# Kernel optimization log

Hardware: AMD Instinct MI355X
Metric: run time of the kernel (lower is better)

## Reference

```python
import jax, jax.numpy as jnp
import numpy as np

N_SU = 8
DATA_DIM = N_SU * N_SU - 1  # 63
BATCH = 1048576


def _gell_mann(n):
    """Generalized Gell-Mann matrices of su(n), Tr(L_a L_b) = 2 delta_ab."""
    mats = []
    for j in range(n):
        for k in range(j + 1, n):
            m = np.zeros((n, n), dtype=np.complex128); m[j, k] = 1.0; m[k, j] = 1.0
            mats.append(m)
            m = np.zeros((n, n), dtype=np.complex128); m[j, k] = -1.0j; m[k, j] = 1.0j
            mats.append(m)
    for l in range(1, n):
        m = np.zeros((n, n), dtype=np.complex128)
        c = np.sqrt(2.0 / (l * (l + 1)))
        for j in range(l):
            m[j, j] = c
        m[l, l] = -l * c
        mats.append(m)
    return np.stack(mats)


def _structure_const(n):
    """f_abc = Tr([L_a,L_b]L_c)/(4i), d_abc = Tr({L_a,L_b}L_c)/4 (both real)."""
    L = _gell_mann(n)                                  # (D, n, n)
    P = np.einsum('aij,bjk->abik', L, L)               # L_a L_b
    comm = P - P.transpose(1, 0, 2, 3)
    anti = P + P.transpose(1, 0, 2, 3)
    f = (np.einsum('abik,cki->abc', comm, L) / 4.0j).real
    d = (np.einsum('abik,cki->abc', anti, L) / 4.0).real
    return f.astype(np.float32), d.astype(np.float32)

F_CONST, D_CONST = _structure_const(N_SU)              # (D, D, D) each, compile-time constants
TRI = np.stack(np.triu_indices(DATA_DIM, 0))           # incl. diagonal
TRI1 = np.stack(np.triu_indices(DATA_DIM, 1))          # strict upper


def setup_inputs() -> dict:
    key = jax.random.key(0)
    k1, k2, k3, k4, k5 = jax.random.split(key, 5)
    D = DATA_DIM
    return {
        'x': jax.random.normal(k1, (BATCH, D), dtype=jnp.float32),
        'r_x': jax.random.uniform(k2, (D * (D + 1) // 2,), dtype=jnp.float32),
        'r_y': jax.random.uniform(k3, (D * (D - 1) // 2,), dtype=jnp.float32),
        'N': jax.random.uniform(k4, (1,), dtype=jnp.float32),
        'omega': jax.random.uniform(k5, (D,), dtype=jnp.float32),
    }


def _forward(x, r_x, r_y, N, omega):
    f = jnp.asarray(F_CONST)
    d = jnp.asarray(D_CONST)
    D = DATA_DIM
    # NOTE: faithful to the torch source, where `v_x = v_y = torch.zeros(...)`
    # aliases ONE tensor: r_y overwrites r_x on the strict upper triangle and
    # v_x is v_y, which makes c_im exactly zero.
    v = jnp.zeros((D, D), dtype=x.dtype)
    v = v.at[TRI[0], TRI[1]].set(r_x)
    v = v.at[TRI1[0], TRI1[1]].set(r_y)
    v_x = v
    v_y = v
    c_re = v_x.T @ v_x + v_y.T @ v_y                   # einsum('ki,kj->ij', v, v) x2
    c_re = c_re / jnp.trace(c_re)
    c_im = v_x.T @ v_y - v_y.T @ v_x                   # exactly zero (aliasing)
    c_re = N * c_re

    # Precompute the small (D,D) superoperator coefficient matrices once, then
    # apply them to the batch with plain matmuls (bn,mn->bm).
    A1 = jnp.einsum('mjk,ij->mik', f, c_re)
    M_re1 = jnp.einsum('mik,nik->mn', A1, f)           # 'mjk,nik,ij->mn'
    A2 = jnp.einsum('mik,ij->mjk', f, c_re)
    M_re2 = jnp.einsum('mjk,njk->mn', A2, f)           # 'mik,njk,ij->mn'
    B1 = jnp.einsum('mjk,ij->mik', f, c_im)
    M_im1 = jnp.einsum('mik,nik->mn', B1, d)
    B2 = jnp.einsum('mik,ij->mjk', f, c_im)
    M_im2 = jnp.einsum('mjk,njk->mn', B2, d)
    M = -2.0 * M_re1 - 2.0 * M_re2 - 2.0 * M_im1 + 2.0 * M_im2

    d_super_x = x @ M.T                                 # (B, D)
    H = 8.0 * jnp.einsum('kij,k->ij', f, omega)
    h_commutator_x = x @ H.T                            # 'kij,k,bj->bi'
    tr_id = -8.0 * jnp.einsum('imj,ij->m', f, c_im)     # (D,), zero here

    S_x = h_commutator_x + d_super_x
    T_x = x + tr_id
    L_x = S_x + T_x
    return x + 0.01 * L_x


def reference(x, r_x, r_y, N, omega):
    return _forward(x, r_x, r_y, N, omega)
```

## Files before the change

kernel.cpp:

```cpp
#include <hip/hip_runtime.h>
#include <hip/hip_bf16.h>

#define DD 63
#define DD2 (DD * DD)
#define NSU 8
#define TROWS 128

typedef __attribute__((ext_vector_type(8))) short short8;
typedef __attribute__((ext_vector_type(4))) float f32x4;

__device__ float  g_F[DD2 * DD];
__device__ float  g_B[DD * DD2];
__device__ float  g_cc[DD2];
__device__ float  g_scale;
__device__ unsigned short g_Gb[64 * 64];

__device__ __forceinline__ unsigned short f2bf(float f) {
    union { float f; unsigned u; } v; v.f = f;
    unsigned r = v.u + 0x7FFFu + ((v.u >> 16) & 1u);
    return (unsigned short)(r >> 16);
}

__device__ __forceinline__ void fill_L(int a, float (*re)[NSU], float (*im)[NSU]) {
    if (a < 56) {
        int p = a >> 1;
        int j = 0, rem = p;
        while (rem >= 7 - j) { rem -= 7 - j; ++j; }
        int k = j + 1 + rem;
        if ((a & 1) == 0) { re[j][k] = 1.f; re[k][j] = 1.f; }
        else             { im[j][k] = -1.f; im[k][j] = 1.f; }
    } else {
        int l = a - 55;
        float c = sqrtf(2.f / (float)(l * (l + 1)));
        for (int j = 0; j < l; ++j) re[j][j] = c;
        re[l][l] = -(float)l * c;
    }
}

__global__ __launch_bounds__(256) void setup_kernel(const float* __restrict__ r_x,
                                                    const float* __restrict__ r_y,
                                                    const float* __restrict__ Np) {
    const int t = threadIdx.x;
    if (blockIdx.x < DD) {
        const int a = blockIdx.x;
        __shared__ float Ar[NSU][NSU], Ai[NSU][NSU];
        __shared__ float Br[4][NSU][NSU], Bi[4][NSU][NSU];
        __shared__ float Cr[4][NSU][NSU], Ci[4][NSU][NSU];
        const int w = t >> 6, lane = t & 63;
        const int r = lane >> 3, c = lane & 7;
        if (t < 64) { Ar[r][c] = 0.f; Ai[r][c] = 0.f; }
        __syncthreads();
        if (t == 0) fill_L(a, Ar, Ai);
        __syncthreads();
        for (int rb = 0; rb < 16; ++rb) {
            const int b = rb * 4 + w;
            const bool act = (b < DD);
            if (act) { Br[w][r][c] = 0.f; Bi[w][r][c] = 0.f; }
            __syncthreads();
            if (act && lane == 0) fill_L(b, Br[w], Bi[w]);
            __syncthreads();
            if (act) {
                float pr = 0.f, pi = 0.f, qr = 0.f, qi = 0.f;
                #pragma unroll
                for (int k = 0; k < NSU; ++k) {
                    pr += Ar[r][k] * Br[w][k][c] - Ai[r][k] * Bi[w][k][c];
                    pi += Ar[r][k] * Bi[w][k][c] + Ai[r][k] * Br[w][k][c];
                    qr += Br[w][r][k] * Ar[k][c] - Bi[w][r][k] * Ai[k][c];
                    qi += Br[w][r][k] * Ai[k][c] + Bi[w][r][k] * Ar[k][c];
                }
                Cr[w][r][c] = pr - qr;
                Ci[w][r][c] = pi - qi;
            }
            __syncthreads();
            if (act && lane < DD) {
                float im;
                if (lane < 56) {
                    int p = lane >> 1;
                    int j = 0, rem = p;
                    while (rem >= 7 - j) { rem -= 7 - j; ++j; }
                    int k = j + 1 + rem;
                    if ((lane & 1) == 0) im = Ci[w][j][k] + Ci[w][k][j];
                    else                 im = Cr[w][j][k] - Cr[w][k][j];
                } else {
                    int l = lane - 55;
                    float cd = sqrtf(2.f / (float)(l * (l + 1)));
                    float s = 0.f;
                    for (int j = 0; j < l; ++j) s += Ci[w][j][j];
                    im = cd * s - (float)l * cd * Ci[w][l][l];
                }
                g_F[(a * DD + b) * DD + lane] = 0.25f * im;
            }
            __syncthreads();
        }
    } else {
        __shared__ float v[DD2];
        __shared__ float ccs[DD2];
        for (int idx = t; idx < DD2; idx += 256) {
            int i = idx / DD, j = idx % DD;
            float val = 0.f;
            if (j > i)       val = r_y[62 * i - (i * (i - 1)) / 2 + (j - i - 1)];
            else if (j == i) val = r_x[63 * i - (i * (i - 1)) / 2];
            v[idx] = val;
        }
        __syncthreads();
        for (int idx = t; idx < DD2; idx += 256) {
            int i = idx / DD, j = idx % DD;
            float s = 0.f;
            for (int k = 0; k < DD; ++k) s = fmaf(v[k * DD + i], v[k * DD + j], s);
            ccs[idx] = s;
            g_cc[idx] = s;
        }
        __syncthreads();
        if (t == 0) {
            float tr = 0.f;
            for (int i = 0; i < DD; ++i) tr += ccs[i * DD + i];
            g_scale = Np[0] / tr;
        }
    }
}

__global__ __launch_bounds__(256) void buildB_kernel() {
    __shared__ float scc[DD2];
    __shared__ float sf[DD2];
    const int t = threadIdx.x;
    const int n = blockIdx.x;
    for (int idx = t; idx < DD2; idx += 256) {
        scc[idx] = g_cc[idx];
        sf[idx]  = g_F[n * DD2 + idx];
    }
    __syncthreads();
    for (int idx = t; idx < DD2; idx += 256) {
        const int j = idx / DD, k = idx % DD;
        float s = 0.f;
        for (int i = 0; i < DD; ++i) s = fmaf(scc[i * DD + j], sf[i * DD + k], s);
        g_B[n * DD2 + idx] = s;
    }
}

__global__ __launch_bounds__(64) void buildKt_kernel(const float* __restrict__ omega) {
    const int m = blockIdx.x >> 6;
    const int n = blockIdx.x & 63;
    const int lane = threadIdx.x;
    if (m >= DD || n >= DD) {
        if (lane == 0) g_Gb[m * 64 + n] = 0;
        return;
    }
    const float* __restrict__ Fm = g_F + m * DD2;
    const float* __restrict__ Bn = g_B + n * DD2;
    float p = 0.f;
    for (int idx = lane; idx < DD2; idx += 64) p = fmaf(Fm[idx], Bn[idx], p);
    float h = (lane < DD) ? g_F[lane * DD2 + m * DD + n] * omega[lane] : 0.f;
    #pragma unroll
    for (int off = 32; off > 0; off >>= 1) {
        p += __shfl_down(p, off);
        h += __shfl_down(h, off);
    }
    if (lane == 0)
        g_Gb[m * 64 + n] = f2bf(0.01f * (-4.f * g_scale * p + 8.f * h));
}

__global__ __launch_bounds__(256, 4) void apply_kernel(const float* __restrict__ x,
                                                       float* __restrict__ out) {
    __shared__ __align__(16) float tile[TROWS * DD];
    __shared__ __align__(16) unsigned short sG[64 * 64];
    const int t = threadIdx.x;
    const size_t base = (size_t)blockIdx.x * (TROWS * DD);

    const float4* __restrict__ gsrc = (const float4*)(x + base);
    float4* __restrict__ ltile = (float4*)tile;
    #pragma unroll
    for (int it = 0; it < 8; ++it) {
        int idx = t + it * 256;
        if (idx < (TROWS * DD / 4)) ltile[idx] = gsrc[idx];
    }
    const int4* __restrict__ gG = (const int4*)g_Gb;
    int4* __restrict__ lG = (int4*)sG;
    lG[t]       = gG[t];
    lG[t + 256] = gG[t + 256];
    __syncthreads();

    const int w = t >> 6, lane = t & 63;
    const int mrow = lane & 15;
    const int q = lane >> 4;

    short8 bfrag[2][4];
    #pragma unroll
    for (int kt = 0; kt < 2; ++kt)
        #pragma unroll
        for (int nt = 0; nt < 4; ++nt)
            bfrag[kt][nt] = *(const short8*)&sG[(nt * 16 + mrow) * 64 + kt * 32 + q * 8];

    #pragma unroll
    for (int mt = 0; mt < 2; ++mt) {
        const int row = w * 32 + mt * 16 + mrow;
        const float* __restrict__ ap = tile + row * DD;
        short8 af[2];
        #pragma unroll
        for (int kt = 0; kt < 2; ++kt)
            #pragma unroll
            for (int j = 0; j < 8; ++j) {
                int k = kt * 32 + q * 8 + j;
                float v = ap[(k == 63) ? 62 : k];
                __hip_bfloat16 h = __float2bfloat16(v);
                af[kt][j] = *reinterpret_cast<short*>(&h);
            }

        f32x4 acc[4] = {{0.f,0.f,0.f,0.f},{0.f,0.f,0.f,0.f},
                        {0.f,0.f,0.f,0.f},{0.f,0.f,0.f,0.f}};
        #pragma unroll
        for (int nt = 0; nt < 4; ++nt) {
            acc[nt] = __builtin_amdgcn_mfma_f32_16x16x32_bf16(af[0], bfrag[0][nt], acc[nt], 0, 0, 0);
            acc[nt] = __builtin_amdgcn_mfma_f32_16x16x32_bf16(af[1], bfrag[1][nt], acc[nt], 0, 0, 0);
        }

        #pragma unroll
        for (int nt = 0; nt < 4; ++nt) {
            const int ocol = nt * 16 + mrow;
            if (ocol < DD) {
                #pragma unroll
                for (int r = 0; r < 4; ++r) {
                    const int orow = w * 32 + mt * 16 + q * 4 + r;
                    const int idx = orow * DD + ocol;
                    tile[idx] = 1.01f * tile[idx] + acc[nt][r];
                }
            }
        }
    }
    __syncthreads();

    float4* __restrict__ gdst = (float4*)(out + base);
    #pragma unroll
    for (int it = 0; it < 8; ++it) {
        int idx = t + it * 256;
        if (idx < (TROWS * DD / 4)) gdst[idx] = ltile[idx];
    }
}

extern "C" void kernel_launch(void* const* d_in, const int* in_sizes, int n_in,
                              void* d_out, int out_size, void* d_ws, size_t ws_size,
                              hipStream_t stream) {
    const float* x     = (const float*)d_in[0];
    const float* r_x   = (const float*)d_in[1];
    const float* r_y   = (const float*)d_in[2];
    const float* Np    = (const float*)d_in[3];
    const float* omega = (const float*)d_in[4];
    float* out = (float*)d_out;

    const int rows = in_sizes[0] / DD;
    const int nblocks = rows / TROWS;

    setup_kernel<<<DD + 1, 256, 0, stream>>>(r_x, r_y, Np);
    buildB_kernel<<<DD, 256, 0, stream>>>();
    buildKt_kernel<<<64 * 64, 64, 0, stream>>>(omega);
    apply_kernel<<<nblocks, 256, 0, stream>>>(x, out);
}
```

Before: 183.8 us.

## Fold residual identity into bf16 operator and write MFMA results directly to global

The 1.01*x residual term is folded into the diagonal of the bf16 operator matrix, so the epilogue stores the MFMA accumulators straight to global memory. This removes the LDS read-modify-write and the second sync-and-copy pass. The x tile is staged into a padded, XOR-swizzled 64-column LDS layout so A fragments can be read with float4 loads. B fragments now come straight from global memory instead of being staged in LDS, and the occupancy hint goes from 4 to 5. In exchange, the identity contribution now passes through bf16 rounding of x, which adds error. The output stores are also scattered per lane rather than written as coalesced float4.

```diff
diff --git a/kernel.cpp b/kernel.cpp
--- a/kernel.cpp
+++ b/kernel.cpp
@@ -156,52 +156,59 @@
         h += __shfl_down(h, off);
     }
     if (lane == 0)
-        g_Gb[m * 64 + n] = f2bf(0.01f * (-4.f * g_scale * p + 8.f * h));
-}
-
-__global__ __launch_bounds__(256, 4) void apply_kernel(const float* __restrict__ x,
+        g_Gb[m * 64 + n] = f2bf(0.01f * (-4.f * g_scale * p + 8.f * h)
+                                + ((m == n) ? 1.01f : 0.f));
+}
+
+__global__ __launch_bounds__(256, 5) void apply_kernel(const float* __restrict__ x,
                                                        float* __restrict__ out) {
-    __shared__ __align__(16) float tile[TROWS * DD];
-    __shared__ __align__(16) unsigned short sG[64 * 64];
+    __shared__ __align__(16) float tile[TROWS * 64];
     const int t = threadIdx.x;
     const size_t base = (size_t)blockIdx.x * (TROWS * DD);
 
-    const float4* __restrict__ gsrc = (const float4*)(x + base);
-    float4* __restrict__ ltile = (float4*)tile;
-    #pragma unroll
-    for (int it = 0; it < 8; ++it) {
-        int idx = t + it * 256;
-        if (idx < (TROWS * DD / 4)) ltile[idx] = gsrc[idx];
-    }
-    const int4* __restrict__ gG = (const int4*)g_Gb;
-    int4* __restrict__ lG = (int4*)sG;
-    lG[t]       = gG[t];
-    lG[t + 256] = gG[t + 256];
+    for (int idx = t; idx < TROWS * DD; idx += 256) {
+        const int row = idx / DD;
+        const int k = idx - row * DD;
+        const int ch = ((k >> 2) ^ (row & 15));
+        tile[row * 64 + ch * 4 + (k & 3)] = x[base + idx];
+    }
+    if (t < TROWS) {
+        const int row = t;
+        tile[row * 64 + ((15 ^ (row & 15)) << 2) + 3] = 0.f;
+    }
     __syncthreads();
 
     const int w = t >> 6, lane = t & 63;
     const int mrow = lane & 15;
     const int q = lane >> 4;
 
+    const short8* __restrict__ gG = (const short8*)g_Gb;
     short8 bfrag[2][4];
     #pragma unroll
     for (int kt = 0; kt < 2; ++kt)
         #pragma unroll
         for (int nt = 0; nt < 4; ++nt)
-            bfrag[kt][nt] = *(const short8*)&sG[(nt * 16 + mrow) * 64 + kt * 32 + q * 8];
+            bfrag[kt][nt] = gG[(nt * 16 + mrow) * 8 + kt * 4 + q];
 
     #pragma unroll
     for (int mt = 0; mt < 2; ++mt) {
         const int row = w * 32 + mt * 16 + mrow;
-        const float* __restrict__ ap = tile + row * DD;
+        const float* __restrict__ rp = tile + row * 64;
+        const int rx = row & 15;
+
+        float va[2][8];
+        #pragma unroll
+        for (int kt = 0; kt < 2; ++kt) {
+            const int c0 = kt * 8 + q * 2;
+            *(float4*)&va[kt][0] = *(const float4*)&rp[((c0 + 0) ^ rx) * 4];
+            *(float4*)&va[kt][4] = *(const float4*)&rp[((c0 + 1) ^ rx) * 4];
+        }
         short8 af[2];
         #pragma unroll
         for (int kt = 0; kt < 2; ++kt)
             #pragma unroll
             for (int j = 0; j < 8; ++j) {
-                int k = kt * 32 + q * 8 + j;
-                float v = ap[(k == 63) ? 62 : k];
-                __hip_bfloat16 h = __float2bfloat16(v);
+                __hip_bfloat16 h = __float2bfloat16(va[kt][j]);
                 af[kt][j] = *reinterpret_cast<short*>(&h);
             }
 
@@ -220,19 +227,10 @@
                 #pragma unroll
                 for (int r = 0; r < 4; ++r) {
                     const int orow = w * 32 + mt * 16 + q * 4 + r;
-                    const int idx = orow * DD + ocol;
-                    tile[idx] = 1.01f * tile[idx] + acc[nt][r];
+                    out[base + orow * DD + ocol] = acc[nt][r];
                 }
             }
         }
-    }
-    __syncthreads();
-
-    float4* __restrict__ gdst = (float4*)(out + base);
-    #pragma unroll
-    for (int it = 0; it < 8; ++it) {
-        int idx = t + it * 256;
-        if (idx < (TROWS * DD / 4)) gdst[idx] = ltile[idx];
     }
 }
 
```

Measured after the change: 206.9 us. 1.13x slower.
